# Performance work log

Measured on AMD Instinct MI355X. Metric: run time of the kernel, lower is better.

## Reference

```python
import jax, jax.numpy as jnp
import numpy as np

BN_EPS = 1e-5


def setup_inputs() -> dict:
    key = jax.random.key(0)
    k1, k2, k3, k4, k5 = jax.random.split(key, 5)
    N, E, D = 100000, 1600000, 128
    x = jax.random.normal(k1, (N, D), dtype=jnp.float32)
    edge_index = jax.random.randint(k2, (2, E), 0, N, dtype=jnp.int64)
    # GCNConv linear weight (PyG stores as [out, in], applied as x @ W.T) + post-agg bias
    W = jax.random.normal(k3, (D, D), dtype=jnp.float32) * (1.0 / np.sqrt(D))
    b = jax.random.normal(k4, (D,), dtype=jnp.float32) * 0.01
    gamma = jnp.ones((D,), dtype=jnp.float32)
    beta = jnp.zeros((D,), dtype=jnp.float32)
    return {"x": x, "edge_index": edge_index, "W": W, "b": b, "gamma": gamma, "beta": beta}


def reference(x, edge_index, W, b, gamma, beta):
    N = x.shape[0]
    src, dst = edge_index[0], edge_index[1]
    # GCN symmetric normalization (no self loops): deg over dst with unit weights
    deg = jax.ops.segment_sum(jnp.ones(src.shape[0], dtype=x.dtype), dst, num_segments=N)
    dinv = jnp.where(deg > 0, jax.lax.rsqrt(jnp.maximum(deg, 1.0)), 0.0)
    norm = dinv[src] * dinv[dst]                      # [E]
    xw = x @ W.T                                      # [N, D] linear transform first (fewer FLOPs)
    msg = xw[src] * norm[:, None]                     # [E, D] gather + scale
    agg = jax.ops.segment_sum(msg, dst, num_segments=N) + b  # [N, D] scatter-add + bias
    # BatchNorm1d over nodes (training-mode batch stats, biased variance)
    mu = jnp.mean(agg, axis=0)
    var = jnp.mean(jnp.square(agg - mu), axis=0)
    h = (agg - mu) * jax.lax.rsqrt(var + BN_EPS) * gamma + beta
    h = jax.nn.relu(h)
    return h + x
```

## Files before the change

### kernel.cpp

```cpp
#include <hip/hip_runtime.h>
#include <hip/hip_bf16.h>

#define DD 128
#define BN_EPS 1e-5f
#define BINSHIFT 8
#define EPB 8192
#define CAP 6144

typedef __attribute__((ext_vector_type(8))) short bf16x8;
typedef __attribute__((ext_vector_type(4))) float f32x4;

static __device__ __forceinline__ size_t rowoff(int r) { return (size_t)r * DD; }

static __device__ __forceinline__ ushort f2bf(float f) {
  __hip_bfloat16 h = __float2bfloat16(f);
  return __builtin_bit_cast(ushort, h);
}
static __device__ __forceinline__ float bf_lo(unsigned u) { return __uint_as_float(u << 16); }
static __device__ __forceinline__ float bf_hi(unsigned u) { return __uint_as_float(u & 0xffff0000u); }

__global__ __launch_bounds__(256) void k_scatter_convw(const int* __restrict__ src,
                                                       const int* __restrict__ dst,
                                                       int* __restrict__ gcursor,
                                                       unsigned* __restrict__ stg,
                                                       const float* __restrict__ W,
                                                       ushort* __restrict__ Wb,
                                                       int E, int NB, int nchunk) {
  int t = threadIdx.x;
  if (blockIdx.x == (unsigned)nchunk) {
#pragma unroll
    for (int i = 0; i < 16; ++i) {
      int f = i * 256 + t;
      int row = f >> 5, c4 = f & 31;
      float4 w = reinterpret_cast<const float4*>(W)[f];
      ushort4 p = make_ushort4(f2bf(w.x), f2bf(w.y), f2bf(w.z), f2bf(w.w));
      int chunk = (c4 >> 1) ^ (row & 7);
      *reinterpret_cast<ushort4*>(reinterpret_cast<char*>(Wb) + row * 256 +
                                  chunk * 16 + (c4 & 1) * 8) = p;
    }
    return;
  }
  __shared__ int hist[1024];
  __shared__ int base[1024];
  long long e0 = (long long)blockIdx.x * EPB;
  int eend = (int)((e0 + EPB < E) ? e0 + EPB : E);
  for (int i = t; i < NB; i += 256) hist[i] = 0;
  __syncthreads();
  for (int i = (int)e0 + t; i < eend; i += 256) atomicAdd(&hist[dst[i] >> BINSHIFT], 1);
  __syncthreads();
  for (int i = t; i < NB; i += 256) {
    int c = hist[i];
    base[i] = c ? (i * CAP + atomicAdd(&gcursor[i], c)) : 0;
    hist[i] = 0;
  }
  __syncthreads();
  for (int i = (int)e0 + t; i < eend; i += 256) {
    int d = dst[i];
    int bin = d >> BINSHIFT;
    unsigned v = ((unsigned)(d & 255) << 24) | (unsigned)src[i];
    int p = atomicAdd(&hist[bin], 1);
    stg[base[bin] + p] = v;
  }
}

__global__ __launch_bounds__(256) void k_binsort(const unsigned* __restrict__ stg,
                                                 const int* __restrict__ gcursor,
                                                 int* __restrict__ ssrc,
                                                 int* __restrict__ offs,
                                                 int* __restrict__ oend,
                                                 float* __restrict__ dinv,
                                                 int N) {
  __shared__ int hist[256];
  __shared__ int scanb[256];
  int b = blockIdx.x;
  int t = threadIdx.x;
  int beg = b * CAP;
  int end = beg + gcursor[b];
  int nloc = N - b * 256;
  if (nloc > 256) nloc = 256;
  hist[t] = 0;
  __syncthreads();
  for (int i = beg + t; i < end; i += 256) atomicAdd(&hist[stg[i] >> 24], 1);
  __syncthreads();
  int h = hist[t];
  scanb[t] = h;
  __syncthreads();
  for (int off = 1; off < 256; off <<= 1) {
    int u = (t >= off) ? scanb[t - off] : 0;
    __syncthreads();
    scanb[t] += u;
    __syncthreads();
  }
  int myexcl = scanb[t] - h;
  __syncthreads();
  scanb[t] = myexcl;
  hist[t] = 0;
  int node = b * 256 + t;
  if (t < nloc) {
    offs[node] = beg + myexcl;
    oend[node] = beg + myexcl + h;
    dinv[node] = h > 0 ? rsqrtf((float)h) : 0.f;
  }
  __syncthreads();
  for (int i = beg + t; i < end; i += 256) {
    unsigned v = stg[i];
    int loc = v >> 24;
    int p = atomicAdd(&hist[loc], 1);
    ssrc[beg + scanb[loc] + p] = (int)(v & 0xFFFFFFu);
  }
}

__global__ __launch_bounds__(256) void k_gemm_mfma(const float* __restrict__ x,
                                                   const ushort* __restrict__ Wb,
                                                   const float* __restrict__ dinv,
                                                   ushort* __restrict__ xwb, int N) {
  __shared__ ushort Abuf[128 * 128];
  __shared__ ushort Bbuf[128 * 128];
  int t = threadIdx.x;
  int brow = blockIdx.x * 128;
  int wid = t >> 6, lane = t & 63;

  {
    const char* gW = reinterpret_cast<const char*>(Wb);
    char* lB = reinterpret_cast<char*>(Bbuf);
#pragma unroll
    for (int i = 0; i < 8; ++i) {
      int off = i * 4096 + wid * 1024;
      __builtin_amdgcn_global_load_lds(
          (const __attribute__((address_space(1))) void*)(gW + off + lane * 16),
          (__attribute__((address_space(3))) void*)(lB + off), 16, 0, 0);
    }
  }
  for (int i = 0; i < 16; ++i) {
    int f = i * 256 + t;
    int row = f >> 5, c4 = f & 31;
    int grow = brow + row;
    float4 v = make_float4(0.f, 0.f, 0.f, 0.f);
    if (grow < N) v = reinterpret_cast<const float4*>(x)[(size_t)grow * 32 + c4];
    ushort4 p = make_ushort4(f2bf(v.x), f2bf(v.y), f2bf(v.z), f2bf(v.w));
    int chunk = (c4 >> 1) ^ (row & 7);
    *reinterpret_cast<ushort4*>(reinterpret_cast<char*>(Abuf) + row * 256 +
                                chunk * 16 + (c4 & 1) * 8) = p;
  }
  __syncthreads();

  int kgrp = lane >> 4;
  int r0 = wid * 32 + (lane & 15);
  int r1 = r0 + 16;
  f32x4 acc[2][8];
#pragma unroll
  for (int rt = 0; rt < 2; ++rt)
#pragma unroll
    for (int cf = 0; cf < 8; ++cf) acc[rt][cf] = (f32x4){0.f, 0.f, 0.f, 0.f};

  const char* Ab = reinterpret_cast<const char*>(Abuf);
  const char* Bb = reinterpret_cast<const char*>(Bbuf);
#pragma unroll
  for (int ks = 0; ks < 4; ++ks) {
    int c = ks * 4 + kgrp;
    bf16x8 a0 = *reinterpret_cast<const bf16x8*>(Ab + r0 * 256 + ((c ^ (r0 & 7)) * 16));
    bf16x8 a1 = *reinterpret_cast<const bf16x8*>(Ab + r1 * 256 + ((c ^ (r1 & 7)) * 16));
#pragma unroll
    for (int cf = 0; cf < 8; ++cf) {
      int bc = cf * 16 + (lane & 15);
      bf16x8 bv = *reinterpret_cast<const bf16x8*>(Bb + bc * 256 + ((c ^ (bc & 7)) * 16));
      acc[0][cf] = __builtin_amdgcn_mfma_f32_16x16x32_bf16(a0, bv, acc[0][cf], 0, 0, 0);
      acc[1][cf] = __builtin_amdgcn_mfma_f32_16x16x32_bf16(a1, bv, acc[1][cf], 0, 0, 0);
    }
  }

#pragma unroll
  for (int rt = 0; rt < 2; ++rt) {
#pragma unroll
    for (int j = 0; j < 4; ++j) {
      int gr = brow + wid * 32 + rt * 16 + (lane >> 4) * 4 + j;
      if (gr < N) {
        float sc = dinv[gr];
        ushort* orow = xwb + (size_t)gr * DD + (lane & 15);
#pragma unroll
        for (int cf = 0; cf < 8; ++cf) orow[cf * 16] = f2bf(acc[rt][cf][j] * sc);
      }
    }
  }
}

__global__ __launch_bounds__(256) void k_aggregate(const int* __restrict__ offs,
                                                   const int* __restrict__ oend,
                                                   const int* __restrict__ ssrc,
                                                   const float* __restrict__ dinv,
                                                   const float* __restrict__ bvec,
                                                   const ushort* __restrict__ xwb,
                                                   float* __restrict__ agg,
                                                   ushort* __restrict__ aggb,
                                                   float* __restrict__ stats, int N) {
  __shared__ float red[1024];
  int t = threadIdx.x;
  int wid = t >> 6, lane = t & 63;
  float bc0 = bvec[2 * lane], bc1 = bvec[2 * lane + 1];
  float s0 = 0.f, q0 = 0.f, s1 = 0.f, q1 = 0.f;
  const unsigned laneb = lane * 2;

  for (int d = blockIdx.x * 4 + wid; d < N; d += gridDim.x * 4) {
    int off = offs[d], end = oend[d];
    float a0 = 0.f, a1 = 0.f, b0 = 0.f, b1 = 0.f;
    float c0 = 0.f, c1 = 0.f, e0 = 0.f, e1 = 0.f;
    int j = off;
    for (; j + 8 <= end; j += 8) {
      int sA = ssrc[j],     sB = ssrc[j + 1], sC = ssrc[j + 2], sD = ssrc[j + 3];
      int sE = ssrc[j + 4], sF = ssrc[j + 5], sG = ssrc[j + 6], sH = ssrc[j + 7];
      unsigned v0 = *reinterpret_cast<const unsigned*>(xwb + (size_t)sA * DD + laneb);
      unsigned v1 = *reinterpret_cast<const unsigned*>(xwb + (size_t)sB * DD + laneb);
      unsigned v2 = *reinterpret_cast<const unsigned*>(xwb + (size_t)sC * DD + laneb);
      unsigned v3 = *reinterpret_cast<const unsigned*>(xwb + (size_t)sD * DD + laneb);
      unsigned v4 = *reinterpret_cast<const unsigned*>(xwb + (size_t)sE * DD + laneb);
      unsigned v5 = *reinterpret_cast<const unsigned*>(xwb + (size_t)sF * DD + laneb);
      unsigned v6 = *reinterpret_cast<const unsigned*>(xwb + (size_t)sG * DD + laneb);
      unsigned v7 = *reinterpret_cast<const unsigned*>(xwb + (size_t)sH * DD + laneb);
      a0 += bf_lo(v0); a1 += bf_hi(v0);
      b0 += bf_lo(v1); b1 += bf_hi(v1);
      c0 += bf_lo(v2); c1 += bf_hi(v2);
      e0 += bf_lo(v3); e1 += bf_hi(v3);
      a0 += bf_lo(v4); a1 += bf_hi(v4);
      b0 += bf_lo(v5); b1 += bf_hi(v5);
      c0 += bf_lo(v6); c1 += bf_hi(v6);
      e0 += bf_lo(v7); e1 += bf_hi(v7);
    }
    if (j + 4 <= end) {
      int sA = ssrc[j], sB = ssrc[j + 1], sC = ssrc[j + 2], sD = ssrc[j + 3];
      unsigned v0 = *reinterpret_cast<const unsigned*>(xwb + (size_t)sA * DD + laneb);
      unsigned v1 = *reinterpret_cast<const unsigned*>(xwb + (size_t)sB * DD + laneb);
      unsigned v2 = *reinterpret_cast<const unsigned*>(xwb + (size_t)sC * DD + laneb);
      unsigned v3 = *reinterpret_cast<const unsigned*>(xwb + (size_t)sD * DD + laneb);
      a0 += bf_lo(v0); a1 += bf_hi(v0);
      b0 += bf_lo(v1); b1 += bf_hi(v1);
      c0 += bf_lo(v2); c1 += bf_hi(v2);
      e0 += bf_lo(v3); e1 += bf_hi(v3);
      j += 4;
    }
    for (; j < end; ++j) {
      int sA = ssrc[j];
      unsigned v0 = *reinterpret_cast<const unsigned*>(xwb + (size_t)sA * DD + laneb);
      a0 += bf_lo(v0); a1 += bf_hi(v0);
    }
    float dd = dinv[d];
    float r0 = ((a0 + b0) + (c0 + e0)) * dd;
    float r1 = ((a1 + b1) + (c1 + e1)) * dd;
    if (aggb) {
      unsigned pk = (unsigned)f2bf(r0) | ((unsigned)f2bf(r1) << 16);
      reinterpret_cast<unsigned*>(aggb + rowoff(d))[lane] = pk;
    } else {
      reinterpret_cast<float2*>(agg + rowoff(d))[lane] = make_float2(r0, r1);
    }
    float t0 = r0 + bc0, t1 = r1 + bc1;
    s0 += t0; q0 += t0 * t0;
    s1 += t1; q1 += t1 * t1;
  }

  float4* rw = reinterpret_cast<float4*>(red);
  rw[wid * 64 + lane] = make_float4(s0, q0, s1, q1);
  __syncthreads();
  {
    float v = red[t] + red[256 + t] + red[512 + t] + red[768 + t];
    int ln = t >> 2, k = t & 3;
    int col = 2 * ln + (k >> 1);
    int rep = blockIdx.x & 7;
    atomicAdd(&stats[rep * 256 + (k & 1) * 128 + col], v);
  }
}

__global__ __launch_bounds__(256) void k_final(float* __restrict__ out,
                                               const ushort* __restrict__ aggb,
                                               const float* __restrict__ x,
                                               const float* __restrict__ b,
                                               const float* __restrict__ gamma,
                                               const float* __restrict__ beta,
                                               const float* __restrict__ stats,
                                               float invN, int N) {
  __shared__ float muS[DD], rsS[DD];
  int t = threadIdx.x;
  if (t < DD) {
    float s = 0.f, q = 0.f;
#pragma unroll
    for (int rep = 0; rep < 8; ++rep) {
      s += stats[rep * 256 + t];
      q += stats[rep * 256 + 128 + t];
    }
    float mu = s * invN;
    float var = q * invN - mu * mu;
    muS[t] = mu;
    rsS[t] = rsqrtf(var + BN_EPS);
  }
  __syncthreads();

  long long i = (long long)blockIdx.x * 256 + threadIdx.x;
  long long stride = (long long)gridDim.x * 256;
  long long total = (long long)N * (DD / 4);
  const float4* __restrict__ x4 = reinterpret_cast<const float4*>(x);
  float4* __restrict__ o4 = reinterpret_cast<float4*>(out);
  const float4* __restrict__ b4 = reinterpret_cast<const float4*>(b);
  const float4* __restrict__ g4 = reinterpret_cast<const float4*>(gamma);
  const float4* __restrict__ be4 = reinterpret_cast<const float4*>(beta);
  const float4* muL = reinterpret_cast<const float4*>(muS);
  const float4* rsL = reinterpret_cast<const float4*>(rsS);
  for (; i < total; i += stride) {
    int c4 = (int)(i & (DD / 4 - 1));
    float4 v;
    if (aggb) {
      uint2 av = reinterpret_cast<const uint2*>(aggb)[i];
      v = make_float4(bf_lo(av.x), bf_hi(av.x), bf_lo(av.y), bf_hi(av.y));
    } else {
      v = o4[i];
    }
    float4 xv = x4[i];
    float4 bb = b4[c4], gg = g4[c4], be = be4[c4], mm = muL[c4], rr = rsL[c4];
    float4 o;
    o.x = fmaxf((v.x + bb.x - mm.x) * rr.x * gg.x + be.x, 0.f) + xv.x;
    o.y = fmaxf((v.y + bb.y - mm.y) * rr.y * gg.y + be.y, 0.f) + xv.y;
    o.z = fmaxf((v.z + bb.z - mm.z) * rr.z * gg.z + be.z, 0.f) + xv.z;
    o.w = fmaxf((v.w + bb.w - mm.w) * rr.w * gg.w + be.w, 0.f) + xv.w;
    o4[i] = o;
  }
}

extern "C" void kernel_launch(void* const* d_in, const int* in_sizes, int n_in,
                              void* d_out, int out_size, void* d_ws, size_t ws_size,
                              hipStream_t stream) {
  const float* x = (const float*)d_in[0];
  const int* ei = (const int*)d_in[1];
  const float* W = (const float*)d_in[2];
  const float* b = (const float*)d_in[3];
  const float* gamma = (const float*)d_in[4];
  const float* beta = (const float*)d_in[5];
  int N = in_sizes[0] / DD;
  int E = in_sizes[1] / 2;
  float* out = (float*)d_out;
  const int* src = ei;
  const int* dst = ei + E;
  int NB = (N + 255) >> BINSHIFT;

  ushort* xwb = (ushort*)d_ws;
  ushort* Wb = xwb + (size_t)N * DD;
  unsigned* stg = (unsigned*)(Wb + DD * DD);
  int* ssrc = (int*)(stg + (size_t)NB * CAP);
  int* offs = ssrc + (size_t)NB * CAP;
  int* oend = offs + N;
  float* dinv = (float*)(oend + N);
  int* gcursor = (int*)(dinv + N);
  float* stats = (float*)(gcursor + 1024);
  ushort* aggb = (ushort*)(stats + 2048);

  size_t need_aggb = (size_t)((char*)(aggb + (size_t)N * DD) - (char*)d_ws);
  if (ws_size < need_aggb) aggb = nullptr;

  hipMemsetAsync(gcursor, 0, 1024 * sizeof(int) + 2048 * sizeof(float), stream);

  int nchunk = (E + EPB - 1) / EPB;
  k_scatter_convw<<<nchunk + 1, 256, 0, stream>>>(src, dst, gcursor, stg, W, Wb,
                                                  E, NB, nchunk);

  k_binsort<<<NB, 256, 0, stream>>>(stg, gcursor, ssrc, offs, oend, dinv, N);

  int gG = (N + 127) / 128;
  k_gemm_mfma<<<gG, 256, 0, stream>>>(x, Wb, dinv, xwb, N);

  k_aggregate<<<2048, 256, 0, stream>>>(offs, oend, ssrc, dinv, b, xwb, out, aggb,
                                        stats, N);

  k_final<<<2048, 256, 0, stream>>>(out, aggb, x, b, gamma, beta, stats,
                                    1.0f / (float)N, N);
}
```

Before: 154.2 us.

## Fuse binsort and GEMM into one launch using global degree counts

Node degrees are now counted with global atomics during the scatter pass, so the GEMM no longer waits on binsort to compute dinv. This lets the binsort and GEMM run as independent blocks of a single merged kernel. The GEMM tile shrinks from 128 to 64 rows per block, which gives more blocks and leaves fewer accumulators per wave. The cost is 1.6M extra global atomics on deg plus a larger memset, in exchange for one fewer kernel launch and overlap of the two phases.

```diff
diff --git a/kernel.cpp b/kernel.cpp
--- a/kernel.cpp
+++ b/kernel.cpp
@@ -23,6 +23,7 @@
                                                        const int* __restrict__ dst,
                                                        int* __restrict__ gcursor,
                                                        unsigned* __restrict__ stg,
+                                                       int* __restrict__ deg,
                                                        const float* __restrict__ W,
                                                        ushort* __restrict__ Wb,
                                                        int E, int NB, int nchunk) {
@@ -46,7 +47,11 @@
   int eend = (int)((e0 + EPB < E) ? e0 + EPB : E);
   for (int i = t; i < NB; i += 256) hist[i] = 0;
   __syncthreads();
-  for (int i = (int)e0 + t; i < eend; i += 256) atomicAdd(&hist[dst[i] >> BINSHIFT], 1);
+  for (int i = (int)e0 + t; i < eend; i += 256) {
+    int d = dst[i];
+    atomicAdd(&hist[d >> BINSHIFT], 1);
+    atomicAdd(&deg[d], 1);
+  }
   __syncthreads();
   for (int i = t; i < NB; i += 256) {
     int c = hist[i];
@@ -63,66 +68,69 @@
   }
 }
 
-__global__ __launch_bounds__(256) void k_binsort(const unsigned* __restrict__ stg,
-                                                 const int* __restrict__ gcursor,
-                                                 int* __restrict__ ssrc,
-                                                 int* __restrict__ offs,
-                                                 int* __restrict__ oend,
-                                                 float* __restrict__ dinv,
-                                                 int N) {
-  __shared__ int hist[256];
-  __shared__ int scanb[256];
-  int b = blockIdx.x;
+__global__ __launch_bounds__(256) void k_gemm_binsort(const float* __restrict__ x,
+                                                      const ushort* __restrict__ Wb,
+                                                      const int* __restrict__ deg,
+                                                      ushort* __restrict__ xwb,
+                                                      const unsigned* __restrict__ stg,
+                                                      const int* __restrict__ gcursor,
+                                                      int* __restrict__ ssrc,
+                                                      int* __restrict__ offs,
+                                                      int* __restrict__ oend,
+                                                      float* __restrict__ dinv,
+                                                      int N, int gG) {
+  __shared__ char pool[49152];
   int t = threadIdx.x;
-  int beg = b * CAP;
-  int end = beg + gcursor[b];
-  int nloc = N - b * 256;
-  if (nloc > 256) nloc = 256;
-  hist[t] = 0;
-  __syncthreads();
-  for (int i = beg + t; i < end; i += 256) atomicAdd(&hist[stg[i] >> 24], 1);
-  __syncthreads();
-  int h = hist[t];
-  scanb[t] = h;
-  __syncthreads();
-  for (int off = 1; off < 256; off <<= 1) {
-    int u = (t >= off) ? scanb[t - off] : 0;
-    __syncthreads();
-    scanb[t] += u;
-    __syncthreads();
-  }
-  int myexcl = scanb[t] - h;
-  __syncthreads();
-  scanb[t] = myexcl;
-  hist[t] = 0;
-  int node = b * 256 + t;
-  if (t < nloc) {
-    offs[node] = beg + myexcl;
-    oend[node] = beg + myexcl + h;
-    dinv[node] = h > 0 ? rsqrtf((float)h) : 0.f;
-  }
-  __syncthreads();
-  for (int i = beg + t; i < end; i += 256) {
-    unsigned v = stg[i];
-    int loc = v >> 24;
-    int p = atomicAdd(&hist[loc], 1);
-    ssrc[beg + scanb[loc] + p] = (int)(v & 0xFFFFFFu);
-  }
-}
-
-__global__ __launch_bounds__(256) void k_gemm_mfma(const float* __restrict__ x,
-                                                   const ushort* __restrict__ Wb,
-                                                   const float* __restrict__ dinv,
-                                                   ushort* __restrict__ xwb, int N) {
-  __shared__ ushort Abuf[128 * 128];
-  __shared__ ushort Bbuf[128 * 128];
-  int t = threadIdx.x;
-  int brow = blockIdx.x * 128;
+
+  if ((int)blockIdx.x >= gG) {
+    int* hist = (int*)pool;
+    int* scanb = (int*)(pool + 1024);
+    int b = blockIdx.x - gG;
+    int beg = b * CAP;
+    int end = beg + gcursor[b];
+    int nloc = N - b * 256;
+    if (nloc > 256) nloc = 256;
+    hist[t] = 0;
+    __syncthreads();
+    for (int i = beg + t; i < end; i += 256) atomicAdd(&hist[stg[i] >> 24], 1);
+    __syncthreads();
+    int h = hist[t];
+    scanb[t] = h;
+    __syncthreads();
+    for (int off = 1; off < 256; off <<= 1) {
+      int u = (t >= off) ? scanb[t - off] : 0;
+      __syncthreads();
+      scanb[t] += u;
+      __syncthreads();
+    }
+    int myexcl = scanb[t] - h;
+    __syncthreads();
+    scanb[t] = myexcl;
+    hist[t] = 0;
+    int node = b * 256 + t;
+    if (t < nloc) {
+      offs[node] = beg + myexcl;
+      oend[node] = beg + myexcl + h;
+      dinv[node] = h > 0 ? rsqrtf((float)h) : 0.f;
+    }
+    __syncthreads();
+    for (int i = beg + t; i < end; i += 256) {
+      unsigned v = stg[i];
+      int loc = v >> 24;
+      int p = atomicAdd(&hist[loc], 1);
+      ssrc[beg + scanb[loc] + p] = (int)(v & 0xFFFFFFu);
+    }
+    return;
+  }
+
+  ushort* Abuf = (ushort*)pool;
+  ushort* Bbuf = (ushort*)(pool + 16384);
+  int brow = blockIdx.x * 64;
   int wid = t >> 6, lane = t & 63;
 
   {
     const char* gW = reinterpret_cast<const char*>(Wb);
-    char* lB = reinterpret_cast<char*>(Bbuf);
+    char* lB = pool + 16384;
 #pragma unroll
     for (int i = 0; i < 8; ++i) {
       int off = i * 4096 + wid * 1024;
@@ -131,7 +139,8 @@
           (__attribute__((address_space(3))) void*)(lB + off), 16, 0, 0);
     }
   }
-  for (int i = 0; i < 16; ++i) {
+#pragma unroll
+  for (int i = 0; i < 8; ++i) {
     int f = i * 256 + t;
     int row = f >> 5, c4 = f & 31;
     int grow = brow + row;
@@ -145,13 +154,10 @@
   __syncthreads();
 
   int kgrp = lane >> 4;
-  int r0 = wid * 32 + (lane & 15);
-  int r1 = r0 + 16;
-  f32x4 acc[2][8];
-#pragma unroll
-  for (int rt = 0; rt < 2; ++rt)
-#pragma unroll
-    for (int cf = 0; cf < 8; ++cf) acc[rt][cf] = (f32x4){0.f, 0.f, 0.f, 0.f};
+  int r0 = wid * 16 + (lane & 15);
+  f32x4 acc[8];
+#pragma unroll
+  for (int cf = 0; cf < 8; ++cf) acc[cf] = (f32x4){0.f, 0.f, 0.f, 0.f};
 
   const char* Ab = reinterpret_cast<const char*>(Abuf);
   const char* Bb = reinterpret_cast<const char*>(Bbuf);
@@ -159,27 +165,23 @@
   for (int ks = 0; ks < 4; ++ks) {
     int c = ks * 4 + kgrp;
     bf16x8 a0 = *reinterpret_cast<const bf16x8*>(Ab + r0 * 256 + ((c ^ (r0 & 7)) * 16));
-    bf16x8 a1 = *reinterpret_cast<const bf16x8*>(Ab + r1 * 256 + ((c ^ (r1 & 7)) * 16));
 #pragma unroll
     for (int cf = 0; cf < 8; ++cf) {
       int bc = cf * 16 + (lane & 15);
       bf16x8 bv = *reinterpret_cast<const bf16x8*>(Bb + bc * 256 + ((c ^ (bc & 7)) * 16));
-      acc[0][cf] = __builtin_amdgcn_mfma_f32_16x16x32_bf16(a0, bv, acc[0][cf], 0, 0, 0);
-      acc[1][cf] = __builtin_amdgcn_mfma_f32_16x16x32_bf16(a1, bv, acc[1][cf], 0, 0, 0);
-    }
-  }
-
-#pragma unroll
-  for (int rt = 0; rt < 2; ++rt) {
-#pragma unroll
-    for (int j = 0; j < 4; ++j) {
-      int gr = brow + wid * 32 + rt * 16 + (lane >> 4) * 4 + j;
-      if (gr < N) {
-        float sc = dinv[gr];
-        ushort* orow = xwb + (size_t)gr * DD + (lane & 15);
-#pragma unroll
-        for (int cf = 0; cf < 8; ++cf) orow[cf * 16] = f2bf(acc[rt][cf][j] * sc);
-      }
+      acc[cf] = __builtin_amdgcn_mfma_f32_16x16x32_bf16(a0, bv, acc[cf], 0, 0, 0);
+    }
+  }
+
+#pragma unroll
+  for (int j = 0; j < 4; ++j) {
+    int gr = brow + wid * 16 + (lane >> 4) * 4 + j;
+    if (gr < N) {
+      int dg = deg[gr];
+      float sc = dg > 0 ? rsqrtf((float)dg) : 0.f;
+      ushort* orow = xwb + (size_t)gr * DD + (lane & 15);
+#pragma unroll
+      for (int cf = 0; cf < 8; ++cf) orow[cf * 16] = f2bf(acc[cf][j] * sc);
     }
   }
 }
@@ -345,23 +347,24 @@
   int* offs = ssrc + (size_t)NB * CAP;
   int* oend = offs + N;
   float* dinv = (float*)(oend + N);
-  int* gcursor = (int*)(dinv + N);
+  int* deg = (int*)(dinv + N);
+  int* gcursor = deg + N;
   float* stats = (float*)(gcursor + 1024);
   ushort* aggb = (ushort*)(stats + 2048);
 
   size_t need_aggb = (size_t)((char*)(aggb + (size_t)N * DD) - (char*)d_ws);
   if (ws_size < need_aggb) aggb = nullptr;
 
-  hipMemsetAsync(gcursor, 0, 1024 * sizeof(int) + 2048 * sizeof(float), stream);
+  hipMemsetAsync(deg, 0, (size_t)N * sizeof(int) + 1024 * sizeof(int) +
+                             2048 * sizeof(float), stream);
 
   int nchunk = (E + EPB - 1) / EPB;
-  k_scatter_convw<<<nchunk + 1, 256, 0, stream>>>(src, dst, gcursor, stg, W, Wb,
-                                                  E, NB, nchunk);
-
-  k_binsort<<<NB, 256, 0, stream>>>(stg, gcursor, ssrc, offs, oend, dinv, N);
-
-  int gG = (N + 127) / 128;
-  k_gemm_mfma<<<gG, 256, 0, stream>>>(x, Wb, dinv, xwb, N);
+  k_scatter_convw<<<nchunk + 1, 256, 0, stream>>>(src, dst, gcursor, stg, deg,
+                                                  W, Wb, E, NB, nchunk);
+
+  int gG = (N + 63) / 64;
+  k_gemm_binsort<<<gG + NB, 256, 0, stream>>>(x, Wb, deg, xwb, stg, gcursor,
+                                              ssrc, offs, oend, dinv, N, gG);
 
   k_aggregate<<<2048, 256, 0, stream>>>(offs, oend, ssrc, dinv, b, xwb, out, aggb,
                                         stats, N);
```

Result: slower. 202.9 us (+31.6%).
